# Kernel tuning notes

Measured on AMD Instinct MI355X. Metric: run time of the kernel, lower is better.

Reference implementation:

```python
import jax, jax.numpy as jnp
import numpy as np

B, T, K, F, H, LH, OUT = 256, 90, 17, 2, 64, 512, 57
N_PER = T * K  # 1530 nodes per graph
IN1 = K * (H + F)  # 1122
CONNS = [[15,13],[13,11],[16,14],[14,12],[11,12],[5,11],[6,12],[5,6],[5,7],[6,8],[7,9],[8,10],[1,2],[0,1],[0,2],[1,3],[2,4],[3,5],[4,6]]

def _build_edge_index():
    temporal = np.array([[i, i + K] for i in range(N_PER - K)], dtype=np.int64).T
    structural = np.array([[a + i * K, b + i * K] for a, b in CONNS for i in range(T)], dtype=np.int64).T
    e = np.concatenate([temporal, structural], axis=1)
    e = np.concatenate([e, e[::-1]], axis=1)  # bidirectional
    e = np.concatenate([e + g * N_PER for g in range(B)], axis=1)  # batch offsets
    return jnp.asarray(e)


def setup_inputs() -> dict:
    key = jax.random.key(0)
    ks = jax.random.split(key, 40)
    def n(i, shape, s=0.05):
        return jax.random.normal(ks[i], shape, dtype=jnp.float32) * s
    inp = {
        'x': jax.random.normal(ks[0], (B * N_PER, F), dtype=jnp.float32),
        'edge_index': _build_edge_index(),
        'gat1_W': n(1, (F, H), 0.3), 'gat1_asrc': n(2, (H,), 0.3), 'gat1_adst': n(3, (H,), 0.3), 'gat1_b': n(4, (H,)),
        'bn1_g': jnp.ones((H,), jnp.float32), 'bn1_b': jnp.zeros((H,), jnp.float32),
        'gat2_W': n(5, (H, H), 0.1), 'gat2_asrc': n(6, (H,), 0.3), 'gat2_adst': n(7, (H,), 0.3), 'gat2_b': n(8, (H,)),
        'bn2_g': jnp.ones((H,), jnp.float32), 'bn2_b': jnp.zeros((H,), jnp.float32),
        'l1f_wih': n(9, (4 * LH, IN1)), 'l1f_whh': n(10, (4 * LH, LH)), 'l1f_bih': n(11, (4 * LH,)), 'l1f_bhh': n(12, (4 * LH,)),
        'l1b_wih': n(13, (4 * LH, IN1)), 'l1b_whh': n(14, (4 * LH, LH)), 'l1b_bih': n(15, (4 * LH,)), 'l1b_bhh': n(16, (4 * LH,)),
        'l2f_wih': n(17, (4 * LH, 2 * LH)), 'l2f_whh': n(18, (4 * LH, LH)), 'l2f_bih': n(19, (4 * LH,)), 'l2f_bhh': n(20, (4 * LH,)),
        'l2b_wih': n(21, (4 * LH, 2 * LH)), 'l2b_whh': n(22, (4 * LH, LH)), 'l2b_bih': n(23, (4 * LH,)), 'l2b_bhh': n(24, (4 * LH,)),
        'h1_w': n(25, (2 * LH, 256)), 'h1_b': n(26, (256,)),
        'h2_w': n(27, (256, OUT)), 'h2_b': n(28, (OUT,)),
    }
    return inp


def _gat(x, src, dst, W, a_src, a_dst, b):
    # PyG GATConv, heads=1, self-loops included in src/dst
    N = x.shape[0]
    xp = x @ W  # [N, H]
    e = jax.nn.leaky_relu((xp @ a_src)[src] + (xp @ a_dst)[dst], 0.2)  # [E]
    m = jax.ops.segment_max(e, dst, num_segments=N)
    w = jnp.exp(e - m[dst])
    den = jax.ops.segment_sum(w, dst, num_segments=N)
    alpha = w / den[dst]
    out = jax.ops.segment_sum(xp[src] * alpha[:, None], dst, num_segments=N)
    return out + b


def _bn(x, g, b):
    mu = x.mean(0)
    var = ((x - mu) ** 2).mean(0)
    return g * (x - mu) * jax.lax.rsqrt(var + 1e-5) + b


def _lstm_dir(x, wih, whh, bih, bhh):
    Bn, Hh = x.shape[0], whh.shape[1]
    def step(carry, xt):
        h, c = carry
        z = xt @ wih.T + h @ whh.T + bih + bhh
        i, f, g, o = jnp.split(z, 4, axis=-1)  # torch gate order
        c = jax.nn.sigmoid(f) * c + jax.nn.sigmoid(i) * jnp.tanh(g)
        h = jax.nn.sigmoid(o) * jnp.tanh(c)
        return (h, c), h
    h0 = jnp.zeros((Bn, Hh), x.dtype)
    _, hs = jax.lax.scan(step, (h0, h0), jnp.swapaxes(x, 0, 1))
    return jnp.swapaxes(hs, 0, 1)


def _bilstm(x, wf_ih, wf_hh, bf_ih, bf_hh, wb_ih, wb_hh, bb_ih, bb_hh):
    fwd = _lstm_dir(x, wf_ih, wf_hh, bf_ih, bf_hh)
    bwd = _lstm_dir(x[:, ::-1], wb_ih, wb_hh, bb_ih, bb_hh)[:, ::-1]
    return jnp.concatenate([fwd, bwd], axis=-1)


def reference(x, edge_index,
              gat1_W, gat1_asrc, gat1_adst, gat1_b, bn1_g, bn1_b,
              gat2_W, gat2_asrc, gat2_adst, gat2_b, bn2_g, bn2_b,
              l1f_wih, l1f_whh, l1f_bih, l1f_bhh, l1b_wih, l1b_whh, l1b_bih, l1b_bhh,
              l2f_wih, l2f_whh, l2f_bih, l2f_bhh, l2b_wih, l2b_whh, l2b_bih, l2b_bhh,
              h1_w, h1_b, h2_w, h2_b):
    N = x.shape[0]
    sl = jnp.arange(N)
    src = jnp.concatenate([edge_index[0], sl])  # add self loops (GATConv default)
    dst = jnp.concatenate([edge_index[1], sl])
    h = jax.nn.relu(_bn(_gat(x, src, dst, gat1_W, gat1_asrc, gat1_adst, gat1_b), bn1_g, bn1_b))
    h = jax.nn.relu(_bn(_gat(h, src, dst, gat2_W, gat2_asrc, gat2_adst, gat2_b), bn2_g, bn2_b))
    feats = jnp.concatenate([h, x], axis=1).reshape(B, T, IN1)  # [B, 90, 1122]
    o = _bilstm(feats, l1f_wih, l1f_whh, l1f_bih, l1f_bhh, l1b_wih, l1b_whh, l1b_bih, l1b_bhh)
    o = _bilstm(o, l2f_wih, l2f_whh, l2f_bih, l2f_bhh, l2b_wih, l2b_whh, l2b_bih, l2b_bhh)
    o = jax.nn.relu(o @ h1_w + h1_b) @ h2_w + h2_b  # [B, 90, 57]
    return o
```

## Files before the change

### kernel.cpp

```cpp
#include <hip/hip_runtime.h>
#include <cstdint>
#include <cstddef>

#define B_    256
#define T_    90
#define K_    17
#define NPER  1530
#define NN    (B_*NPER)
#define H_    64
#define LH    512
#define G4    2048
#define IN1   1122
#define IN1P  1152
#define SEQR  (B_*T_)
#define OUT_  57

typedef unsigned short u16;
typedef __attribute__((ext_vector_type(8))) short short8;
typedef __attribute__((ext_vector_type(4))) float f32x4;

__device__ __forceinline__ float b2f(u16 u){ union{unsigned i; float f;} x; x.i=((unsigned)u)<<16; return x.f; }
__device__ __forceinline__ u16 f2b(float f){ union{float f; unsigned i;} x; x.f=f; unsigned r=x.i+0x7fffu+((x.i>>16)&1u); return (u16)(r>>16); }
__device__ __forceinline__ float sigm(float v){ return 1.f/(1.f+__expf(-v)); }
__device__ __forceinline__ float tanh_(float v){ return 2.f*sigm(2.f*v)-1.f; }

__global__ __launch_bounds__(256)
void stg_sentinel(float* __restrict__ out, int n){
  int i=blockIdx.x*256+threadIdx.x;
  if(i<n) out[i]=123.0f;
}

__global__ __launch_bounds__(256)
void stg_permute_w(const float* __restrict__ src, u16* __restrict__ dst, int Ks, int Kd){
  size_t idx=(size_t)blockIdx.x*256+threadIdx.x;
  int rn=(int)(idx/Kd), kk=(int)(idx%Kd);
  int j=rn>>2, G=rn&3, ro=G*LH+j;
  dst[idx] = (kk<Ks)? f2b(src[(size_t)ro*Ks+kk]) : (u16)0;
}

__global__ __launch_bounds__(256)
void stg_prep_bias(const float* __restrict__ bih, const float* __restrict__ bhh, float* __restrict__ dst){
  int rn=blockIdx.x*256+threadIdx.x;
  int j=rn>>2, G=rn&3, ro=G*LH+j;
  dst[rn]=bih[ro]+bhh[ro];
}

__global__ __launch_bounds__(256)
void stg_transpose_pad(const float* __restrict__ src, u16* __restrict__ dst, int R, int C, int Crows){
  size_t idx=(size_t)blockIdx.x*256+threadIdx.x;
  int c=(int)(idx/R), r=(int)(idx%R);
  dst[idx] = (c<C)? f2b(src[(size_t)r*C+c]) : (u16)0;
  (void)Crows;
}

__global__ __launch_bounds__(256)
void stg_gat1_xp(const float* __restrict__ x, const float* __restrict__ W, u16* __restrict__ xp){
  size_t idx=(size_t)blockIdx.x*256+threadIdx.x;
  size_t n=idx>>6; int c=idx&63;
  float v=x[n*2]*W[c]+x[n*2+1]*W[64+c];
  xp[idx]=f2b(v);
}

__global__ __launch_bounds__(256)
void stg_scores(const u16* __restrict__ xp, const float* __restrict__ as, const float* __restrict__ ad,
                float* __restrict__ ssrc, float* __restrict__ sdst){
  const int lane=threadIdx.x&63;
  const size_t n=(size_t)blockIdx.x*4+(threadIdx.x>>6);
  float v=b2f(xp[n*64+lane]);
  float s1=v*as[lane], s2=v*ad[lane];
  #pragma unroll
  for(int m=1;m<64;m<<=1){ s1+=__shfl_xor(s1,m); s2+=__shfl_xor(s2,m); }
  if(lane==0){ ssrc[n]=s1; sdst[n]=s2; }
}

__constant__ int c_deg[17]={2,3,3,2,2,4,4,2,2,1,1,3,3,2,2,1,1};
__constant__ int c_adj[17][4]={{1,2,0,0},{2,0,3,0},{1,0,4,0},{1,5,0,0},{2,6,0,0},
 {11,6,7,3},{12,5,8,4},{5,9,0,0},{6,10,0,0},{7,0,0,0},{8,0,0,0},
 {13,12,5,0},{14,11,6,0},{15,11,0,0},{16,12,0,0},{13,0,0,0},{14,0,0,0}};

__global__ __launch_bounds__(256)
void stg_gat_agg(const u16* __restrict__ xp, const float* __restrict__ ssrc, const float* __restrict__ sdst,
                 const float* __restrict__ bias, u16* __restrict__ out){
  const int lane=threadIdx.x&63;
  const int n=blockIdx.x*4+(threadIdx.x>>6);
  const int r=n%NPER, t=r/K_, k=r%K_;
  const int dg=c_deg[k];
  const int base=n-k;
  const int nb0=n;
  const int nb1=(t>0)?      n-K_ : n;  const bool v1=(t>0);
  const int nb2=(t<T_-1)?   n+K_ : n;  const bool v2=(t<T_-1);
  const int nb3=base+c_adj[k][0];
  const int nb4=base+c_adj[k][1];      const bool v4=(dg>1);
  const int nb5=base+c_adj[k][2];      const bool v5=(dg>2);
  const int nb6=base+c_adj[k][3];      const bool v6=(dg>3);
  const float sd=sdst[n];
  const float NEG=-1e30f;
  auto lrelu=[](float v){ return v>0.f? v : 0.2f*v; };
  float e0=lrelu(ssrc[nb0]+sd);
  float e1=v1? lrelu(ssrc[nb1]+sd) : NEG;
  float e2=v2? lrelu(ssrc[nb2]+sd) : NEG;
  float e3=    lrelu(ssrc[nb3]+sd);
  float e4=v4? lrelu(ssrc[nb4]+sd) : NEG;
  float e5=v5? lrelu(ssrc[nb5]+sd) : NEG;
  float e6=v6? lrelu(ssrc[nb6]+sd) : NEG;
  float mx=fmaxf(fmaxf(fmaxf(e0,e1),fmaxf(e2,e3)),fmaxf(fmaxf(e4,e5),e6));
  float w0=__expf(e0-mx), w1=__expf(e1-mx), w2=__expf(e2-mx), w3=__expf(e3-mx);
  float w4=__expf(e4-mx), w5=__expf(e5-mx), w6=__expf(e6-mx);
  const float inv=1.f/(w0+w1+w2+w3+w4+w5+w6);
  float acc = w0*b2f(xp[(size_t)nb0*64+lane])
            + w1*b2f(xp[(size_t)nb1*64+lane])
            + w2*b2f(xp[(size_t)nb2*64+lane])
            + w3*b2f(xp[(size_t)nb3*64+lane])
            + w4*b2f(xp[(size_t)nb4*64+lane])
            + w5*b2f(xp[(size_t)nb5*64+lane])
            + w6*b2f(xp[(size_t)nb6*64+lane]);
  out[(size_t)n*64+lane]=f2b(acc*inv+bias[lane]);
}

__global__ __launch_bounds__(256)
void stg_bn_part(const u16* __restrict__ in, float* __restrict__ part){
  const int c=threadIdx.x&63, sub=threadIdx.x>>6;
  float s=0.f,q=0.f;
  for(size_t n=(size_t)blockIdx.x*4+sub; n<NN; n+=1024){
    float v=b2f(in[n*64+c]); s+=v; q+=v*v;
  }
  __shared__ float sS[4][64], sQ[4][64];
  sS[sub][c]=s; sQ[sub][c]=q;
  __syncthreads();
  if(sub==0){
    float a=0,bq=0;
    for(int i=0;i<4;i++){a+=sS[i][c]; bq+=sQ[i][c];}
    part[blockIdx.x*128+c*2]=a; part[blockIdx.x*128+c*2+1]=bq;
  }
}

__global__ void stg_bn_fin(const float* __restrict__ part, const float* __restrict__ g,
                           const float* __restrict__ b, float* __restrict__ stats){
  const int c=threadIdx.x;
  float s=0,q=0;
  for(int p=0;p<256;++p){ s+=part[p*128+c*2]; q+=part[p*128+c*2+1]; }
  const float invN=1.f/(float)NN;
  float mu=s*invN, var=q*invN-mu*mu;
  float istd=rsqrtf(var+1e-5f);
  float a=g[c]*istd;
  stats[c*2]=a; stats[c*2+1]=b[c]-mu*a;
}

__global__ __launch_bounds__(256)
void stg_bn_apply(const u16* __restrict__ in, const float* __restrict__ stats, u16* __restrict__ out){
  size_t idx=(size_t)blockIdx.x*256+threadIdx.x;
  int c=idx&63;
  float v=b2f(in[idx])*stats[c*2]+stats[c*2+1];
  out[idx]=f2b(fmaxf(v,0.f));
}

__global__ __launch_bounds__(256)
void stg_build_feats(const u16* __restrict__ h2, const float* __restrict__ x, u16* __restrict__ feats){
  size_t idx=(size_t)blockIdx.x*256+threadIdx.x;
  size_t row=idx/IN1P; int cc=(int)(idx%IN1P);
  u16 outv=0;
  if(cc<IN1){
    int k=cc/66, f=cc%66;
    size_t g=row/T_, t=row%T_;
    size_t node=g*NPER+t*K_+k;
    outv = (f<64)? h2[node*64+f] : f2b(x[node*2+(f-64)]);
  }
  feats[idx]=outv;
}

template<int BM,int BN,int EPI>
__global__ __launch_bounds__(256)
void stg_gemm_bt(const u16* __restrict__ A, int ldA,
                 const u16* __restrict__ Bt, int ldB,
                 void* __restrict__ Cp, int ldC, int K,
                 const float* __restrict__ bias)
{
  constexpr int WM=BM/2, WN=BN/2, FM=WM/16, FN=WN/16;
  __shared__ u16 As[BM*32];
  __shared__ u16 Bs[BN*32];
  const int tid=threadIdx.x, w=tid>>6, lane=tid&63;
  const int wr=w>>1, wc=w&1;
  const size_t row0=(size_t)blockIdx.x*BM;
  const size_t col0=(size_t)blockIdx.y*BN;
  f32x4 acc[FM][FN];
  #pragma unroll
  for(int i=0;i<FM;i++)
    #pragma unroll
    for(int j=0;j<FN;j++)
      #pragma unroll
      for(int r=0;r<4;r++) acc[i][j][r]=0.f;

  for(int k0=0;k0<K;k0+=32){
    #pragma unroll
    for(int q=0;q<BM/64;++q){
      const int is=w*(BM/64)+q;
      const u16* gp=A+(row0+is*16+(lane>>2))*(size_t)ldA+k0+(lane&3)*8;
      *(short8*)&As[is*512+lane*8]=*(const short8*)gp;
    }
    #pragma unroll
    for(int q=0;q<BN/64;++q){
      const int is=w*(BN/64)+q;
      const u16* gp=Bt+(col0+is*16+(lane>>2))*(size_t)ldB+k0+(lane&3)*8;
      *(short8*)&Bs[is*512+lane*8]=*(const short8*)gp;
    }
    __syncthreads();
    short8 af[FM], bf[FN];
    #pragma unroll
    for(int mi=0;mi<FM;mi++)
      af[mi]=*(const short8*)&As[(wr*WM+mi*16+(lane&15))*32+(lane>>4)*8];
    #pragma unroll
    for(int ni=0;ni<FN;ni++)
      bf[ni]=*(const short8*)&Bs[(wc*WN+ni*16+(lane&15))*32+(lane>>4)*8];
    #pragma unroll
    for(int mi=0;mi<FM;mi++)
      #pragma unroll
      for(int ni=0;ni<FN;ni++)
        acc[mi][ni]=__builtin_amdgcn_mfma_f32_16x16x32_bf16(af[mi],bf[ni],acc[mi][ni],0,0,0);
    __syncthreads();
  }
  #pragma unroll
  for(int mi=0;mi<FM;mi++)
   #pragma unroll
   for(int ni=0;ni<FN;ni++)
    #pragma unroll
    for(int r=0;r<4;r++){
      const size_t row=row0+wr*WM+mi*16+(lane>>4)*4+r;
      const size_t col=col0+wc*WN+ni*16+(lane&15);
      float v=acc[mi][ni][r];
      if constexpr (EPI==0){ ((u16*)Cp)[row*ldC+col]=f2b(v); }
      else if constexpr (EPI==1){ v+=bias[col]; ((u16*)Cp)[row*ldC+col]=f2b(fmaxf(v,0.f)); }
      else { if(col<OUT_){ ((float*)Cp)[row*ldC+col]=v+bias[col]; } }
    }
}

__global__ __launch_bounds__(512)
void stg_lstm_step(const u16* __restrict__ hprev, u16* __restrict__ hcur,
                   float* __restrict__ cst,
                   const u16* __restrict__ whh,
                   const u16* __restrict__ xpf, const u16* __restrict__ xpb,
                   const float* __restrict__ bias,
                   u16* __restrict__ seq,
                   int t)
{
  __shared__ u16 As[2][2*2048];
  __shared__ u16 Bs[2][2*2048];
  __shared__ float Zs[64*64];
  const int dir = blockIdx.z;
  const int tt  = dir ? (T_-1-t) : t;
  const u16* xp = dir ? xpb : xpf;
  const u16* Ap = hprev + (size_t)dir*B_*LH;
  const u16* Bp = whh   + (size_t)dir*G4*LH;
  const int tid=threadIdx.x, w=tid>>6, lane=tid&63;
  const int wr=w>>2, wc=w&3;
  const int row0=blockIdx.x*64, col0=blockIdx.y*64;

  const int gc_ = col0 + wc*16 + (lane&15);
  const float bias_v = bias[dir*G4 + gc_];
  u16 xpr_[2][4];
  #pragma unroll
  for(int mi=0;mi<2;mi++)
    #pragma unroll
    for(int r=0;r<4;r++){
      const int b=row0+wr*32+mi*16+(lane>>4)*4+r;
      xpr_[mi][r]=xp[(size_t)(b*T_+tt)*G4+gc_];
    }
  const int rlA=tid>>4,        uA=tid&15;
  const int rlB=(tid+512)>>4,  uB=tid&15;
  const size_t ciA=(size_t)dir*B_*LH + (size_t)(row0+rlA)*LH + (col0>>2)+uA;
  const size_t ciB=(size_t)dir*B_*LH + (size_t)(row0+rlB)*LH + (col0>>2)+uB;
  const float cprevA=cst[ciA];
  const float cprevB=cst[ciB];

  const int sp=w>>2, ss=w&3;
  const int srow=ss*16+(lane>>2);
  const int scO=(lane&3)*8;
  const u16* gA = Ap + (size_t)(row0+srow)*LH + sp*32 + scO;
  const u16* gB = Bp + (size_t)(col0+srow)*LH + sp*32 + scO;
  const int lA = sp*2048 + srow*32 + scO;

  f32x4 acc[2];
  #pragma unroll
  for(int i=0;i<2;i++)
    #pragma unroll
    for(int r=0;r<4;r++) acc[i][r]=0.f;

  short8 ra=*(const short8*)(gA);
  short8 rb=*(const short8*)(gB);
  *(short8*)&As[0][lA]=ra; *(short8*)&Bs[0][lA]=rb;

  int cur=0;
  for(int it=0; it<8; ++it){
    if(it<7){ ra=*(const short8*)(gA+(it+1)*64); rb=*(const short8*)(gB+(it+1)*64); }
    __syncthreads();
    #pragma unroll
    for(int p=0;p<2;++p){
      short8 af[2], bf;
      #pragma unroll
      for(int mi=0;mi<2;mi++)
        af[mi]=*(const short8*)&As[cur][p*2048+(wr*32+mi*16+(lane&15))*32+(lane>>4)*8];
      bf=*(const short8*)&Bs[cur][p*2048+(wc*16+(lane&15))*32+(lane>>4)*8];
      #pragma unroll
      for(int mi=0;mi<2;mi++)
        acc[mi]=__builtin_amdgcn_mfma_f32_16x16x32_bf16(af[mi],bf,acc[mi],0,0,0);
    }
    if(it<7){ *(short8*)&As[cur^1][lA]=ra; *(short8*)&Bs[cur^1][lA]=rb; }
    cur^=1;
  }
  #pragma unroll
  for(int mi=0;mi<2;mi++)
    #pragma unroll
    for(int r=0;r<4;r++){
      const int rl=wr*32+mi*16+(lane>>4)*4+r;
      const int cl=wc*16+(lane&15);
      Zs[rl*64+cl]=acc[mi][r] + b2f(xpr_[mi][r]) + bias_v;
    }
  __syncthreads();
  {
    const float zi=Zs[rlA*64+4*uA+0], zf=Zs[rlA*64+4*uA+1];
    const float zg=Zs[rlA*64+4*uA+2], zo=Zs[rlA*64+4*uA+3];
    float c = sigm(zf)*cprevA + sigm(zi)*tanh_(zg);
    cst[ciA]=c;
    float h = sigm(zo)*tanh_(c);
    hcur[ciA]=f2b(h);
    seq[(size_t)((row0+rlA)*T_+tt)*(2*LH) + (size_t)dir*LH + (col0>>2)+uA]=f2b(h);
  }
  {
    const float zi=Zs[rlB*64+4*uB+0], zf=Zs[rlB*64+4*uB+1];
    const float zg=Zs[rlB*64+4*uB+2], zo=Zs[rlB*64+4*uB+3];
    float c = sigm(zf)*cprevB + sigm(zi)*tanh_(zg);
    cst[ciB]=c;
    float h = sigm(zo)*tanh_(c);
    hcur[ciB]=f2b(h);
    seq[(size_t)((row0+rlB)*T_+tt)*(2*LH) + (size_t)dir*LH + (col0>>2)+uB]=f2b(h);
  }
}

extern "C" void kernel_launch(void* const* d_in, const int* in_sizes, int n_in,
                              void* d_out, int out_size, void* d_ws, size_t ws_size,
                              hipStream_t stream)
{
  (void)in_sizes; (void)n_in;
  const float* x    =(const float*)d_in[0];
  const float* g1W  =(const float*)d_in[2];
  const float* g1as =(const float*)d_in[3];
  const float* g1ad =(const float*)d_in[4];
  const float* g1b  =(const float*)d_in[5];
  const float* bn1g =(const float*)d_in[6];
  const float* bn1b =(const float*)d_in[7];
  const float* g2W  =(const float*)d_in[8];
  const float* g2as =(const float*)d_in[9];
  const float* g2ad =(const float*)d_in[10];
  const float* g2b  =(const float*)d_in[11];
  const float* bn2g =(const float*)d_in[12];
  const float* bn2b =(const float*)d_in[13];
  const float* l1f_wih=(const float*)d_in[14];
  const float* l1f_whh=(const float*)d_in[15];
  const float* l1f_bih=(const float*)d_in[16];
  const float* l1f_bhh=(const float*)d_in[17];
  const float* l1b_wih=(const float*)d_in[18];
  const float* l1b_whh=(const float*)d_in[19];
  const float* l1b_bih=(const float*)d_in[20];
  const float* l1b_bhh=(const float*)d_in[21];
  const float* l2f_wih=(const float*)d_in[22];
  const float* l2f_whh=(const float*)d_in[23];
  const float* l2f_bih=(const float*)d_in[24];
  const float* l2f_bhh=(const float*)d_in[25];
  const float* l2b_wih=(const float*)d_in[26];
  const float* l2b_whh=(const float*)d_in[27];
  const float* l2b_bih=(const float*)d_in[28];
  const float* l2b_bhh=(const float*)d_in[29];
  const float* h1w  =(const float*)d_in[30];
  const float* h1b  =(const float*)d_in[31];
  const float* h2w  =(const float*)d_in[32];
  const float* h2b  =(const float*)d_in[33];

  const size_t SZ_w1ih  = (size_t)G4*IN1P*2;
  const size_t SZ_w2ih  = (size_t)G4*1024*2;
  const size_t SZ_whh   = (size_t)4*G4*LH*2;
  const size_t SZ_bias  = (size_t)4*G4*4;
  const size_t SZ_w2gT  = (size_t)64*64*2;
  const size_t SZ_h1T   = (size_t)256*1024*2;
  const size_t SZ_h2T   = (size_t)64*256*2;
  const size_t SZ_part  = (size_t)256*128*4;
  const size_t SZ_stats = (size_t)64*2*4;
  const size_t SZ_hs    = (size_t)2*B_*LH*2;
  const size_t SZ_cs    = (size_t)2*B_*LH*4;
  const size_t SZ_xpr   = (size_t)SEQR*G4*2;
  const size_t SZ_R12   = 2*SZ_xpr;
  const size_t SZ_feats = (size_t)SEQR*IN1P*2;
  const size_t SZ_gat   = (size_t)NN*64*2;
  const size_t SZ_sc    = (size_t)NN*4;

  char* base=(char*)d_ws; size_t o=0;
  auto take=[&](size_t b)->size_t{ size_t r=o; o=(o+b+255)&~(size_t)255; return r; };
  const size_t off_w1ih = take(2*SZ_w1ih);
  const size_t off_whh  = take(SZ_whh);
  const size_t off_bias = take(SZ_bias);
  const size_t off_w2gT = take(SZ_w2gT);
  const size_t off_h1T  = take(SZ_h1T);
  const size_t off_h2T  = take(SZ_h2T);
  const size_t off_part = take(SZ_part);
  const size_t off_stat = take(SZ_stats);
  const size_t off_hs0  = take(SZ_hs);
  const size_t off_hs1  = take(SZ_hs);
  const size_t off_cs   = take(SZ_cs);
  const size_t off_R12  = take(SZ_R12);
  const size_t off_R3   = take(SZ_feats);
  const size_t NEED = o;
  if (NEED > ws_size) {
    stg_sentinel<<<(out_size+255)/256,256,0,stream>>>((float*)d_out, out_size);
    return;
  }

  u16* w1ihF=(u16*)(base+off_w1ih);
  u16* w1ihB=(u16*)(base+off_w1ih+SZ_w1ih);
  u16* w2ihF=(u16*)(base+off_w1ih);
  u16* w2ihB=(u16*)(base+off_w1ih+SZ_w2ih);
  u16* whhAll=(u16*)(base+off_whh);
  float* biasAll=(float*)(base+off_bias);
  u16* w2gT=(u16*)(base+off_w2gT);
  u16* h1T =(u16*)(base+off_h1T);
  u16* h2T =(u16*)(base+off_h2T);
  float* part=(float*)(base+off_part);
  float* stats=(float*)(base+off_stat);
  u16* hs0=(u16*)(base+off_hs0);
  u16* hs1=(u16*)(base+off_hs1);
  float* cs=(float*)(base+off_cs);
  u16* xprF=(u16*)(base+off_R12);
  u16* xprB=(u16*)(base+off_R12+SZ_xpr);
  u16* xpB_=(u16*)(base+off_R12);
  u16* aggB=(u16*)(base+off_R12+SZ_gat);
  u16* hB  =(u16*)(base+off_R12+2*SZ_gat);
  float* ssrc=(float*)(base+off_R12+3*SZ_gat);
  float* sdst=(float*)(base+off_R12+3*SZ_gat+SZ_sc);
  u16* mid =(u16*)(base+off_R12);
  u16* feats=(u16*)(base+off_R3);
  u16* seq  =(u16*)(base+off_R3);

  stg_permute_w<<<G4*IN1P/256,256,0,stream>>>(l1f_wih,w1ihF,IN1,IN1P);
  stg_permute_w<<<G4*IN1P/256,256,0,stream>>>(l1b_wih,w1ihB,IN1,IN1P);
  stg_permute_w<<<G4*LH/256,256,0,stream>>>(l1f_whh,whhAll+0*(size_t)G4*LH,LH,LH);
  stg_permute_w<<<G4*LH/256,256,0,stream>>>(l1b_whh,whhAll+1*(size_t)G4*LH,LH,LH);
  stg_permute_w<<<G4*LH/256,256,0,stream>>>(l2f_whh,whhAll+2*(size_t)G4*LH,LH,LH);
  stg_permute_w<<<G4*LH/256,256,0,stream>>>(l2b_whh,whhAll+3*(size_t)G4*LH,LH,LH);
  stg_prep_bias<<<G4/256,256,0,stream>>>(l1f_bih,l1f_bhh,biasAll+0*G4);
  stg_prep_bias<<<G4/256,256,0,stream>>>(l1b_bih,l1b_bhh,biasAll+1*G4);
  stg_prep_bias<<<G4/256,256,0,stream>>>(l2f_bih,l2f_bhh,biasAll+2*G4);
  stg_prep_bias<<<G4/256,256,0,stream>>>(l2b_bih,l2b_bhh,biasAll+3*G4);
  stg_transpose_pad<<<64*64/256,256,0,stream>>>(g2W,w2gT,64,64,64);
  stg_transpose_pad<<<256*1024/256,256,0,stream>>>(h1w,h1T,1024,256,256);
  stg_transpose_pad<<<64*256/256,256,0,stream>>>(h2w,h2T,256,57,64);

  stg_gat1_xp<<<NN*64/256,256,0,stream>>>(x,g1W,xpB_);
  stg_scores<<<NN/4,256,0,stream>>>(xpB_,g1as,g1ad,ssrc,sdst);
  stg_gat_agg<<<NN/4,256,0,stream>>>(xpB_,ssrc,sdst,g1b,aggB);
  stg_bn_part<<<256,256,0,stream>>>(aggB,part);
  stg_bn_fin<<<1,64,0,stream>>>(part,bn1g,bn1b,stats);
  stg_bn_apply<<<NN*64/256,256,0,stream>>>(aggB,stats,hB);

  stg_gemm_bt<128,64,0><<<dim3(NN/128,1),256,0,stream>>>(hB,64,w2gT,64,xpB_,64,64,nullptr);
  stg_scores<<<NN/4,256,0,stream>>>(xpB_,g2as,g2ad,ssrc,sdst);
  stg_gat_agg<<<NN/4,256,0,stream>>>(xpB_,ssrc,sdst,g2b,aggB);
  stg_bn_part<<<256,256,0,stream>>>(aggB,part);
  stg_bn_fin<<<1,64,0,stream>>>(part,bn2g,bn2b,stats);
  stg_bn_apply<<<NN*64/256,256,0,stream>>>(aggB,stats,hB);

  stg_build_feats<<<SEQR*IN1P/256,256,0,stream>>>(hB,x,feats);

  stg_gemm_bt<128,128,0><<<dim3(SEQR/128,G4/128),256,0,stream>>>(feats,IN1P,w1ihF,IN1P,xprF,G4,IN1P,nullptr);
  stg_gemm_bt<128,128,0><<<dim3(SEQR/128,G4/128),256,0,stream>>>(feats,IN1P,w1ihB,IN1P,xprB,G4,IN1P,nullptr);
  stg_permute_w<<<G4*1024/256,256,0,stream>>>(l2f_wih,w2ihF,1024,1024);
  stg_permute_w<<<G4*1024/256,256,0,stream>>>(l2b_wih,w2ihB,1024,1024);

  hipMemsetAsync(hs0,0,SZ_hs,stream);
  hipMemsetAsync(cs,0,SZ_cs,stream);
  for(int t=0;t<T_;++t){
    u16* hp=(t&1)?hs1:hs0; u16* hc=(t&1)?hs0:hs1;
    stg_lstm_step<<<dim3(B_/64,G4/64,2),512,0,stream>>>(hp,hc,cs,whhAll,xprF,xprB,biasAll,seq,t);
  }

  stg_gemm_bt<128,128,0><<<dim3(SEQR/128,G4/128),256,0,stream>>>(seq,1024,w2ihF,1024,xprF,G4,1024,nullptr);
  stg_gemm_bt<128,128,0><<<dim3(SEQR/128,G4/128),256,0,stream>>>(seq,1024,w2ihB,1024,xprB,G4,1024,nullptr);
  hipMemsetAsync(hs0,0,SZ_hs,stream);
  hipMemsetAsync(cs,0,SZ_cs,stream);
  for(int t=0;t<T_;++t){
    u16* hp=(t&1)?hs1:hs0; u16* hc=(t&1)?hs0:hs1;
    stg_lstm_step<<<dim3(B_/64,G4/64,2),512,0,stream>>>(hp,hc,cs,whhAll+(size_t)2*G4*LH,xprF,xprB,biasAll+2*G4,seq,t);
  }

  stg_gemm_bt<128,128,1><<<dim3(SEQR/128,256/128),256,0,stream>>>(seq,1024,h1T,1024,mid,256,1024,h1b);
  stg_gemm_bt<128,64,2><<<dim3(SEQR/128,1),256,0,stream>>>(mid,256,h2T,256,d_out,OUT_,256,h2b);
}
```

Before: 2.542 ms.

## Double-buffer LDS tiles in bf16 GEMM with register prefetch of next K slice

The GEMM kernel now keeps two LDS buffers for the A and B tiles. It loads the next K slice from global memory into registers while the MFMAs run on the current buffer, then writes those registers into the other buffer. This removes one __syncthreads per iteration and hides global-load latency behind compute. In exchange it doubles LDS use and adds register pressure, which may lower occupancy.

```diff
diff --git a/kernel.cpp b/kernel.cpp
--- a/kernel.cpp
+++ b/kernel.cpp
@@ -175,9 +175,9 @@
                  void* __restrict__ Cp, int ldC, int K,
                  const float* __restrict__ bias)
 {
-  constexpr int WM=BM/2, WN=BN/2, FM=WM/16, FN=WN/16;
-  __shared__ u16 As[BM*32];
-  __shared__ u16 Bs[BN*32];
+  constexpr int WM=BM/2, WN=BN/2, FM=WM/16, FN=WN/16, QA=BM/64, QB=BN/64;
+  __shared__ u16 As[2][BM*32];
+  __shared__ u16 Bs[2][BN*32];
   const int tid=threadIdx.x, w=tid>>6, lane=tid&63;
   const int wr=w>>1, wc=w&1;
   const size_t row0=(size_t)blockIdx.x*BM;
@@ -190,33 +190,60 @@
       #pragma unroll
       for(int r=0;r<4;r++) acc[i][j][r]=0.f;
 
-  for(int k0=0;k0<K;k0+=32){
-    #pragma unroll
-    for(int q=0;q<BM/64;++q){
-      const int is=w*(BM/64)+q;
-      const u16* gp=A+(row0+is*16+(lane>>2))*(size_t)ldA+k0+(lane&3)*8;
-      *(short8*)&As[is*512+lane*8]=*(const short8*)gp;
-    }
-    #pragma unroll
-    for(int q=0;q<BN/64;++q){
-      const int is=w*(BN/64)+q;
-      const u16* gp=Bt+(col0+is*16+(lane>>2))*(size_t)ldB+k0+(lane&3)*8;
-      *(short8*)&Bs[is*512+lane*8]=*(const short8*)gp;
+  const int srow=lane>>2, scO=(lane&3)*8;
+  const u16* gA[QA]; const u16* gB[QB]; int lA_[QA], lB_[QB];
+  #pragma unroll
+  for(int q=0;q<QA;++q){
+    const int is=w*QA+q;
+    gA[q]=A+(row0+is*16+srow)*(size_t)ldA+scO;
+    lA_[q]=is*512+lane*8;
+  }
+  #pragma unroll
+  for(int q=0;q<QB;++q){
+    const int is=w*QB+q;
+    gB[q]=Bt+(col0+is*16+srow)*(size_t)ldB+scO;
+    lB_[q]=is*512+lane*8;
+  }
+
+  short8 ra[QA], rb[QB];
+  #pragma unroll
+  for(int q=0;q<QA;++q) ra[q]=*(const short8*)(gA[q]);
+  #pragma unroll
+  for(int q=0;q<QB;++q) rb[q]=*(const short8*)(gB[q]);
+  #pragma unroll
+  for(int q=0;q<QA;++q) *(short8*)&As[0][lA_[q]]=ra[q];
+  #pragma unroll
+  for(int q=0;q<QB;++q) *(short8*)&Bs[0][lB_[q]]=rb[q];
+
+  const int nIter=K/32;
+  int cur=0;
+  for(int it=0; it<nIter; ++it){
+    if(it<nIter-1){
+      #pragma unroll
+      for(int q=0;q<QA;++q) ra[q]=*(const short8*)(gA[q]+(it+1)*32);
+      #pragma unroll
+      for(int q=0;q<QB;++q) rb[q]=*(const short8*)(gB[q]+(it+1)*32);
     }
     __syncthreads();
     short8 af[FM], bf[FN];
     #pragma unroll
     for(int mi=0;mi<FM;mi++)
-      af[mi]=*(const short8*)&As[(wr*WM+mi*16+(lane&15))*32+(lane>>4)*8];
+      af[mi]=*(const short8*)&As[cur][(wr*WM+mi*16+(lane&15))*32+(lane>>4)*8];
     #pragma unroll
     for(int ni=0;ni<FN;ni++)
-      bf[ni]=*(const short8*)&Bs[(wc*WN+ni*16+(lane&15))*32+(lane>>4)*8];
+      bf[ni]=*(const short8*)&Bs[cur][(wc*WN+ni*16+(lane&15))*32+(lane>>4)*8];
     #pragma unroll
     for(int mi=0;mi<FM;mi++)
       #pragma unroll
       for(int ni=0;ni<FN;ni++)
         acc[mi][ni]=__builtin_amdgcn_mfma_f32_16x16x32_bf16(af[mi],bf[ni],acc[mi][ni],0,0,0);
-    __syncthreads();
+    if(it<nIter-1){
+      #pragma unroll
+      for(int q=0;q<QA;++q) *(short8*)&As[cur^1][lA_[q]]=ra[q];
+      #pragma unroll
+      for(int q=0;q<QB;++q) *(short8*)&Bs[cur^1][lB_[q]]=rb[q];
+    }
+    cur^=1;
   }
   #pragma unroll
   for(int mi=0;mi<FM;mi++)
```

After: 2.500 ms. About the same (-1.6%).
